# Kernel tuning notes

Hardware: AMD Instinct MI355X
Metric: run time of the kernel (lower is better)

## Reference

```python
import jax, jax.numpy as jnp
import numpy as np

PATCH = 768
POS = 64
HID = 512
B, N = 8, 2048


def setup_inputs() -> dict:
    key = jax.random.key(0)
    ks = jax.random.split(key, 8)
    d_in = PATCH + POS
    s = 1.0 / np.sqrt(d_in)
    return {
        "patches": jax.random.normal(ks[0], (B, N, PATCH), jnp.float32),
        "positions": jax.random.normal(ks[1], (B, N, POS), jnp.float32),
        "Wq": jax.random.uniform(ks[2], (d_in, HID), jnp.float32, -s, s),
        "bq": jax.random.uniform(ks[3], (HID,), jnp.float32, -s, s),
        "Wk": jax.random.uniform(ks[4], (d_in, HID), jnp.float32, -s, s),
        "bk": jax.random.uniform(ks[5], (d_in and HID,), jnp.float32, -s, s),
        "Wv": jax.random.uniform(ks[6], (d_in, HID), jnp.float32, -s, s),
        "bv": jax.random.uniform(ks[7], (HID,), jnp.float32, -s, s),
    }


def reference(patches, positions, Wq, bq, Wk, bk, Wv, bv):
    # concat patch features with positional features: [B, N, PATCH+POS]
    x = jnp.concatenate([patches, positions], axis=-1)
    Q = x @ Wq + bq  # [B, N, HID]
    K = x @ Wk + bk
    V = x @ Wv + bv
    scale = jnp.sqrt(jnp.asarray(HID, x.dtype))
    scores = jnp.einsum("bnd,bmd->bnm", Q, K) / scale  # [B, N, N]
    weights = jax.nn.softmax(scores, axis=-1)
    return jnp.einsum("bnm,bmd->bnd", weights, V)  # [B, N, HID]
```

## Files before the change

kernel.cpp:

```cpp
#include <hip/hip_runtime.h>
#include <hip/hip_bf16.h>
#include <math.h>

typedef __hip_bfloat16 bf16;
typedef __attribute__((ext_vector_type(4))) float f32x4;
typedef __attribute__((ext_vector_type(8))) short s16x8;

typedef const __attribute__((address_space(1))) void gvoid_t;
typedef __attribute__((address_space(3))) void lvoid_t;

__device__ __forceinline__ void gload16(const void* g, void* l) {
  __builtin_amdgcn_global_load_lds((gvoid_t*)g, (lvoid_t*)l, 16, 0, 0);
}
__device__ __forceinline__ unsigned short f2b(float f) {
  bf16 h = __float2bfloat16(f);
  return *(unsigned short*)&h;
}

__global__ __launch_bounds__(256) void prep_x(const float* __restrict__ patches,
                                              const float* __restrict__ positions,
                                              bf16* __restrict__ xb) {
  const long long row = blockIdx.x;
  const int c = threadIdx.x;
  const bool lo = (c < 192);
  const bool hi = (c >= 192) && (c < 208);
  const float* src = lo ? (patches + row * 768 + c * 4)
                        : (positions + row * 64 + (c - 192) * 4);
  if (lo || hi) {
    float4 v = *(const float4*)src;
    const int dst = lo ? (c * 4) : (768 + (c - 192) * 4);
    uint2 w;
    w.x = (unsigned int)f2b(v.x) | ((unsigned int)f2b(v.y) << 16);
    w.y = (unsigned int)f2b(v.z) | ((unsigned int)f2b(v.w) << 16);
    *(uint2*)(xb + row * 832 + dst) = w;
  }
}

__global__ __launch_bounds__(256) void prep_w(const float* __restrict__ Wq,
                                              const float* __restrict__ Wk,
                                              const float* __restrict__ Wv,
                                              bf16* __restrict__ Wt) {
  __shared__ float tile[32][33];
  const int z = blockIdx.z;
  const float* W = (z == 0) ? Wq : (z == 1) ? Wk : Wv;
  bf16* T = Wt + (long long)z * 512 * 832;
  const int n0 = blockIdx.x * 32;
  const int k0 = blockIdx.y * 32;
  const int tx = threadIdx.x, ty = threadIdx.y;
  #pragma unroll
  for (int i = 0; i < 32; i += 8)
    tile[ty + i][tx] = W[(long long)(k0 + ty + i) * 512 + n0 + tx];
  __syncthreads();
  #pragma unroll
  for (int i = 0; i < 32; i += 8)
    T[(long long)(n0 + ty + i) * 832 + k0 + tx] = __float2bfloat16(tile[tx][ty + i]);
}

#define VMW8  asm volatile("s_waitcnt vmcnt(8)" ::: "memory")
#define VMW10 asm volatile("s_waitcnt vmcnt(10)" ::: "memory")
#define PBAR do { __builtin_amdgcn_s_barrier(); __builtin_amdgcn_sched_barrier(0); } while (0)

__device__ __forceinline__ void stage_half(const bf16* src, char* lds, int stride) {
  gload16(src, lds);
  gload16(src + 64 * stride, lds + 8192);
}
__device__ __forceinline__ void lda4(const bf16* base, int rowbase, int llo,
                                     int xk0, int xk1, s16x8 af[4][2]) {
  #pragma unroll
  for (int mf = 0; mf < 4; mf++) {
    const bf16* p = base + (rowbase + mf * 16 + llo) * 64;
    af[mf][0] = *(const s16x8*)(p + xk0);
    af[mf][1] = *(const s16x8*)(p + xk1);
  }
}
__device__ __forceinline__ void ldb2(const bf16* base, int rowbase, int llo,
                                     int xk0, int xk1, s16x8 bfr[2][2]) {
  #pragma unroll
  for (int nf = 0; nf < 2; nf++) {
    const bf16* p = base + (rowbase + nf * 16 + llo) * 64;
    bfr[nf][0] = *(const s16x8*)(p + xk0);
    bfr[nf][1] = *(const s16x8*)(p + xk1);
  }
}
__device__ __forceinline__ void mma16(f32x4 acc[4][2], s16x8 af[4][2],
                                      s16x8 bfr[2][2]) {
  __builtin_amdgcn_s_setprio(1);
  #pragma unroll
  for (int mf = 0; mf < 4; mf++)
    #pragma unroll
    for (int nf = 0; nf < 2; nf++) {
      acc[mf][nf] = __builtin_amdgcn_mfma_f32_16x16x32_bf16(
          af[mf][0], bfr[nf][0], acc[mf][nf], 0, 0, 0);
      acc[mf][nf] = __builtin_amdgcn_mfma_f32_16x16x32_bf16(
          af[mf][1], bfr[nf][1], acc[mf][nf], 0, 0, 0);
    }
  __builtin_amdgcn_s_setprio(0);
}

__global__ __launch_bounds__(512, 2) void gemm_qkv(
    const bf16* __restrict__ xb, const bf16* __restrict__ Wt,
    const float* __restrict__ bq, const float* __restrict__ bk,
    const float* __restrict__ bv,
    bf16* __restrict__ qk, bf16* __restrict__ vt) {
  __shared__ bf16 As[2][256 * 64];
  __shared__ bf16 Bs[2][256 * 64];
  const int tid = threadIdx.x;
  const int wave = tid >> 6, lane = tid & 63;
  const int llo = lane & 15, lhi = lane >> 4;
  const int wm = wave >> 2, wn = wave & 3;

  const unsigned int lin = blockIdx.x;
  const unsigned int xcd = lin & 7u, idx = lin >> 3;
  const unsigned int g = xcd * 48u + idx;
  const unsigned int bm_t = g / 6u;
  const unsigned int bn_t = g - bm_t * 6u;
  const int row0 = (int)bm_t * 256;
  const int col0 = (int)bn_t * 256;
  const int z = col0 >> 9;

  const int sr = tid >> 3;
  const int kkofs = ((tid & 7) ^ (sr & 7)) << 3;
  const bf16* sA = xb + (long long)(row0 + sr) * 832 + kkofs;
  const bf16* sB = Wt + (long long)(col0 + sr) * 832 + kkofs;
  const int wofs = wave * 1024;

  const int xk0 = ((lhi ^ (llo & 7)) << 3);
  const int xk1 = (((4 + lhi) ^ (llo & 7)) << 3);

  f32x4 acc[2][2][4][2] = {};
  s16x8 af[4][2], bf0[2][2], bf1[2][2];

  stage_half(sA, (char*)As[0] + wofs, 832);
  stage_half(sB, (char*)Bs[0] + wofs, 832);
  stage_half(sB + 128 * 832, (char*)Bs[0] + 16384 + wofs, 832);
  stage_half(sA + 128 * 832, (char*)As[0] + 16384 + wofs, 832);
  stage_half(sA + 64, (char*)As[1] + wofs, 832);
  stage_half(sB + 64, (char*)Bs[1] + wofs, 832);
  VMW8; PBAR;

  for (int i = 0; i < 6; ++i) {
    const int kt1 = (2 * i + 1) * 64;
    const int kt2 = (2 * i + 2 <= 12) ? (2 * i + 2) * 64 : 768;
    const int kt3 = (2 * i + 3 <= 12) ? (2 * i + 3) * 64 : 768;
    lda4(As[0], wm * 64, llo, xk0, xk1, af);
    ldb2(Bs[0], wn * 32, llo, xk0, xk1, bf0);
    stage_half(sB + 128 * 832 + kt1, (char*)Bs[1] + 16384 + wofs, 832);
    VMW8; PBAR;
    mma16(acc[0][0], af, bf0);
    ldb2(Bs[0], 128 + wn * 32, llo, xk0, xk1, bf1);
    stage_half(sA + 128 * 832 + kt1, (char*)As[1] + 16384 + wofs, 832);
    VMW8; PBAR;
    mma16(acc[0][1], af, bf1);
    lda4(As[0], 128 + wm * 64, llo, xk0, xk1, af);
    stage_half(sA + kt2, (char*)As[0] + wofs, 832);
    PBAR;
    mma16(acc[1][0], af, bf0);
    stage_half(sB + kt2, (char*)Bs[0] + wofs, 832);
    VMW8; PBAR;
    mma16(acc[1][1], af, bf1);
    lda4(As[1], wm * 64, llo, xk0, xk1, af);
    ldb2(Bs[1], wn * 32, llo, xk0, xk1, bf0);
    stage_half(sB + 128 * 832 + kt2, (char*)Bs[0] + 16384 + wofs, 832);
    VMW8; PBAR;
    mma16(acc[0][0], af, bf0);
    ldb2(Bs[1], 128 + wn * 32, llo, xk0, xk1, bf1);
    stage_half(sA + 128 * 832 + kt2, (char*)As[0] + 16384 + wofs, 832);
    VMW8; PBAR;
    mma16(acc[0][1], af, bf1);
    lda4(As[1], 128 + wm * 64, llo, xk0, xk1, af);
    stage_half(sA + kt3, (char*)As[1] + wofs, 832);
    PBAR;
    mma16(acc[1][0], af, bf0);
    stage_half(sB + kt3, (char*)Bs[1] + wofs, 832);
    VMW8; PBAR;
    mma16(acc[1][1], af, bf1);
  }

  asm volatile("s_waitcnt vmcnt(4)" ::: "memory");
  PBAR;
  lda4(As[0], wm * 64, llo, xk0, xk1, af);
  ldb2(Bs[0], wn * 32, llo, xk0, xk1, bf0);
  ldb2(Bs[0], 128 + wn * 32, llo, xk0, xk1, bf1);
  mma16(acc[0][0], af, bf0);
  mma16(acc[0][1], af, bf1);
  lda4(As[0], 128 + wm * 64, llo, xk0, xk1, af);
  mma16(acc[1][0], af, bf0);
  mma16(acc[1][1], af, bf1);
  asm volatile("s_waitcnt vmcnt(0)" ::: "memory");

  if (z < 2) {
    const float* bias = z ? bk : bq;
    bf16* outp = qk + (long long)z * 16384 * 512;
    #pragma unroll
    for (int qr = 0; qr < 2; qr++)
      #pragma unroll
      for (int qc = 0; qc < 2; qc++)
        #pragma unroll
        for (int mf = 0; mf < 4; mf++)
          #pragma unroll
          for (int nf = 0; nf < 2; nf++) {
            const int c = (col0 & 511) + qc * 128 + wn * 32 + nf * 16 + llo;
            const int grow0 = row0 + qr * 128 + wm * 64 + mf * 16 + lhi * 4;
            const float bb = bias[c];
            #pragma unroll
            for (int r = 0; r < 4; r++)
              outp[(long long)(grow0 + r) * 512 + c] =
                  __float2bfloat16(acc[qr][qc][mf][nf][r] + bb);
          }
  } else {
    #pragma unroll
    for (int qr = 0; qr < 2; qr++)
      #pragma unroll
      for (int qc = 0; qc < 2; qc++)
        #pragma unroll
        for (int mf = 0; mf < 4; mf++)
          #pragma unroll
          for (int nf = 0; nf < 2; nf++) {
            const int c = (col0 & 511) + qc * 128 + wn * 32 + nf * 16 + llo;
            const int grow0 = row0 + qr * 128 + wm * 64 + mf * 16 + lhi * 4;
            const int b = grow0 >> 11, j = grow0 & 2047;
            const float bb = bv[c];
            uint2 w;
            w.x = (unsigned int)f2b(acc[qr][qc][mf][nf][0] + bb) |
                  ((unsigned int)f2b(acc[qr][qc][mf][nf][1] + bb) << 16);
            w.y = (unsigned int)f2b(acc[qr][qc][mf][nf][2] + bb) |
                  ((unsigned int)f2b(acc[qr][qc][mf][nf][3] + bb) << 16);
            *(uint2*)(vt + (long long)b * 512 * 2048 + (long long)c * 2048 + j) = w;
          }
  }
}

__global__ __launch_bounds__(512, 2) void gemm_scores(const bf16* __restrict__ qk,
                                                      bf16* __restrict__ S,
                                                      float* __restrict__ rowsumP) {
  __shared__ bf16 As[2][256 * 64];
  __shared__ bf16 Bs[2][256 * 64];
  const int tid = threadIdx.x;
  const int wave = tid >> 6, lane = tid & 63;
  const int llo = lane & 15, lhi = lane >> 4;
  const int wm = wave >> 2, wn = wave & 3;

  const unsigned int lin = blockIdx.x;
  const int b = (int)(lin & 7u);
  const unsigned int idx = lin >> 3;
  const int row0 = (int)(idx >> 3) * 256;
  const int coltile = (int)(idx & 7u);
  const int col0 = coltile * 256;

  const bf16* Ab = qk + (long long)b * 2048 * 512;
  const bf16* Bb = qk + (long long)16384 * 512 + (long long)b * 2048 * 512;

  const int sr = tid >> 3;
  const int kkofs = ((tid & 7) ^ (sr & 7)) << 3;
  const bf16* sA = Ab + (long long)(row0 + sr) * 512 + kkofs;
  const bf16* sB = Bb + (long long)(col0 + sr) * 512 + kkofs;
  const int wofs = wave * 1024;

  const int xk0 = ((lhi ^ (llo & 7)) << 3);
  const int xk1 = (((4 + lhi) ^ (llo & 7)) << 3);

  f32x4 acc[2][2][4][2] = {};
  s16x8 af[4][2], bf0[2][2], bf1[2][2];

  stage_half(sA, (char*)As[0] + wofs, 512);
  stage_half(sB, (char*)Bs[0] + wofs, 512);
  stage_half(sB + 128 * 512, (char*)Bs[0] + 16384 + wofs, 512);
  stage_half(sA + 128 * 512, (char*)As[0] + 16384 + wofs, 512);
  stage_half(sA + 64, (char*)As[1] + wofs, 512);
  stage_half(sB + 64, (char*)Bs[1] + wofs, 512);
  VMW8; PBAR;

  for (int i = 0; i < 4; ++i) {
    const int kt1 = (2 * i + 1) * 64;
    const int kt2 = (2 * i + 2 < 8) ? (2 * i + 2) * 64 : 448;
    const int kt3 = (2 * i + 3 < 8) ? (2 * i + 3) * 64 : 448;
    lda4(As[0], wm * 64, llo, xk0, xk1, af);
    ldb2(Bs[0], wn * 32, llo, xk0, xk1, bf0);
    stage_half(sB + 128 * 512 + kt1, (char*)Bs[1] + 16384 + wofs, 512);
    VMW8; PBAR;
    mma16(acc[0][0], af, bf0);
    ldb2(Bs[0], 128 + wn * 32, llo, xk0, xk1, bf1);
    stage_half(sA + 128 * 512 + kt1, (char*)As[1] + 16384 + wofs, 512);
    VMW8; PBAR;
    mma16(acc[0][1], af, bf1);
    lda4(As[0], 128 + wm * 64, llo, xk0, xk1, af);
    stage_half(sA + kt2, (char*)As[0] + wofs, 512);
    PBAR;
    mma16(acc[1][0], af, bf0);
    stage_half(sB + kt2, (char*)Bs[0] + wofs, 512);
    VMW8; PBAR;
    mma16(acc[1][1], af, bf1);
    lda4(As[1], wm * 64, llo, xk0, xk1, af);
    ldb2(Bs[1], wn * 32, llo, xk0, xk1, bf0);
    stage_half(sB + 128 * 512 + kt2, (char*)Bs[0] + 16384 + wofs, 512);
    VMW8; PBAR;
    mma16(acc[0][0], af, bf0);
    ldb2(Bs[1], 128 + wn * 32, llo, xk0, xk1, bf1);
    stage_half(sA + 128 * 512 + kt2, (char*)As[0] + 16384 + wofs, 512);
    VMW8; PBAR;
    mma16(acc[0][1], af, bf1);
    lda4(As[1], 128 + wm * 64, llo, xk0, xk1, af);
    stage_half(sA + kt3, (char*)As[1] + wofs, 512);
    PBAR;
    mma16(acc[1][0], af, bf0);
    stage_half(sB + kt3, (char*)Bs[1] + wofs, 512);
    VMW8; PBAR;
    mma16(acc[1][1], af, bf1);
  }

  __syncthreads();

  const float alpha = 0.044194173824159216f;
  bf16* Sb = S + (long long)b * 2048 * 2048;
  #pragma unroll
  for (int qr = 0; qr < 2; qr++)
    #pragma unroll
    for (int qc = 0; qc < 2; qc++)
      #pragma unroll
      for (int mf = 0; mf < 4; mf++)
        #pragma unroll
        for (int nf = 0; nf < 2; nf++) {
          #pragma unroll
          for (int r = 0; r < 4; r++)
            acc[qr][qc][mf][nf][r] = __expf(acc[qr][qc][mf][nf][r] * alpha);
          const int gcol = col0 + qc * 128 + wn * 32 + nf * 16 + llo;
          const int grow0 = row0 + qr * 128 + wm * 64 + mf * 16 + lhi * 4;
          #pragma unroll
          for (int r = 0; r < 4; r++)
            Sb[(long long)(grow0 + r) * 2048 + gcol] =
                __float2bfloat16(acc[qr][qc][mf][nf][r]);
        }

  float* psum = (float*)As;
  #pragma unroll
  for (int qr = 0; qr < 2; qr++)
    #pragma unroll
    for (int mf = 0; mf < 4; mf++)
      #pragma unroll
      for (int r = 0; r < 4; r++) {
        float p = acc[qr][0][mf][0][r] + acc[qr][0][mf][1][r] +
                  acc[qr][1][mf][0][r] + acc[qr][1][mf][1][r];
        p += __shfl_xor(p, 1, 64);
        p += __shfl_xor(p, 2, 64);
        p += __shfl_xor(p, 4, 64);
        p += __shfl_xor(p, 8, 64);
        if (llo == 0)
          psum[wn * 256 + qr * 128 + wm * 64 + mf * 16 + lhi * 4 + r] = p;
      }
  __syncthreads();
  if (tid < 256) {
    const float v = psum[tid] + psum[256 + tid] + psum[512 + tid] + psum[768 + tid];
    rowsumP[(long long)(b * 8 + coltile) * 2048 + row0 + tid] = v;
  }
}

__global__ __launch_bounds__(256) void reduce_rowsum(
    const float* __restrict__ rowsumP, float* __restrict__ rinv) {
  const int i = blockIdx.x * 256 + threadIdx.x;
  const int b = i >> 11, row = i & 2047;
  const float* p = rowsumP + ((long long)b * 8) * 2048 + row;
  float s = 0.f;
  #pragma unroll
  for (int t = 0; t < 8; t++) s += p[t * 2048];
  rinv[i] = 1.0f / s;
}

#define PV_TILE(c, cs, kstage)                                              \
  do {                                                                      \
                                                              \
    lda4(As3[c], wm * 64, llo, xk0, xk1, af);                               \
    ldb2(Bs3[c], wn * 32, llo, xk0, xk1, bfr);                              \
    stage_half(sA + (kstage), (char*)As3[cs] + wofs, 2048);                 \
    stage_half(sB + (kstage), (char*)Bs3[cs] + wofs, 2048);                 \
    VMW10; PBAR;                                                            \
    mma16(acc[0], af, bfr);                                                 \
                              \
    lda4(As3[c], 128 + wm * 64, llo, xk0, xk1, af);                         \
    stage_half(sA + 128 * 2048 + (kstage), (char*)As3[cs] + 16384 + wofs,   \
               2048);                                                       \
    VMW8; PBAR;                                                             \
    mma16(acc[1], af, bfr);                                                 \
  } while (0)

__global__ __launch_bounds__(512, 2) void gemm_pv(const bf16* __restrict__ S,
                                                  const bf16* __restrict__ vt,
                                                  const float* __restrict__ rinv,
                                                  float* __restrict__ out) {
  __shared__ bf16 As3[3][256 * 64];
  __shared__ bf16 Bs3[3][128 * 64];
  const int tid = threadIdx.x;
  const int wave = tid >> 6, lane = tid & 63;
  const int llo = lane & 15, lhi = lane >> 4;
  const int wm = wave >> 2, wn = wave & 3;

  const unsigned int lin = blockIdx.x;
  const int b = (int)(lin & 7u);
  const unsigned int idx = lin >> 3;
  const int row0 = (int)(idx >> 2) * 256;
  const int col0 = (int)(idx & 3u) * 128;

  const bf16* Ab = S + (long long)b * 2048 * 2048;
  const bf16* Bb = vt + (long long)b * 512 * 2048;

  const int sr = tid >> 3;
  const int kkofs = ((tid & 7) ^ (sr & 7)) << 3;
  const bf16* sA = Ab + (long long)(row0 + sr) * 2048 + kkofs;
  const bf16* sB = Bb + (long long)(col0 + sr) * 2048 + kkofs;
  const int wofs = wave * 1024;

  const int xk0 = ((lhi ^ (llo & 7)) << 3);
  const int xk1 = (((4 + lhi) ^ (llo & 7)) << 3);

  f32x4 acc[2][4][2] = {};
  s16x8 af[4][2], bfr[2][2];

  stage_half(sA, (char*)As3[0] + wofs, 2048);
  stage_half(sB, (char*)Bs3[0] + wofs, 2048);
  stage_half(sA + 128 * 2048, (char*)As3[0] + 16384 + wofs, 2048);
  stage_half(sA + 64, (char*)As3[1] + wofs, 2048);
  stage_half(sB + 64, (char*)Bs3[1] + wofs, 2048);
  stage_half(sA + 128 * 2048 + 64, (char*)As3[1] + 16384 + wofs, 2048);
  VMW8; PBAR;

  for (int j = 0; j < 10; ++j) {
    const int kb = j * 192;
    PV_TILE(0, 2, kb + 128);
    PV_TILE(1, 0, kb + 192);
    PV_TILE(2, 1, kb + 256);
  }
  PV_TILE(0, 2, 1984);
  PV_TILE(1, 0, 1984);

  asm volatile("s_waitcnt vmcnt(0)" ::: "memory");

  const float* rs = rinv + (long long)b * 2048;
  float* Ob = out + (long long)b * 2048 * 512;
  #pragma unroll
  for (int qr = 0; qr < 2; qr++)
    #pragma unroll
    for (int mf = 0; mf < 4; mf++) {
      const int grow0 = row0 + qr * 128 + wm * 64 + mf * 16 + lhi * 4;
      float iv[4];
      #pragma unroll
      for (int r = 0; r < 4; r++) iv[r] = rs[grow0 + r];
      #pragma unroll
      for (int nf = 0; nf < 2; nf++) {
        const int gcol = col0 + wn * 32 + nf * 16 + llo;
        #pragma unroll
        for (int r = 0; r < 4; r++)
          Ob[(long long)(grow0 + r) * 512 + gcol] = acc[qr][mf][nf][r] * iv[r];
      }
    }
}
#undef PV_TILE

extern "C" void kernel_launch(void* const* d_in, const int* in_sizes, int n_in,
                              void* d_out, int out_size, void* d_ws, size_t ws_size,
                              hipStream_t stream) {
  const float* patches = (const float*)d_in[0];
  const float* positions = (const float*)d_in[1];
  const float* Wq = (const float*)d_in[2];
  const float* bq = (const float*)d_in[3];
  const float* Wk = (const float*)d_in[4];
  const float* bk = (const float*)d_in[5];
  const float* Wv = (const float*)d_in[6];
  const float* bv = (const float*)d_in[7];
  float* out = (float*)d_out;

  if (ws_size < 149422080u) return;

  char* ws = (char*)d_ws;
  bf16* Wt = (bf16*)(ws);
  bf16* xb = (bf16*)(ws + 2555904);
  bf16* qk = (bf16*)(ws + 29818880);
  bf16* vt = (bf16*)(ws + 63373312);
  bf16* S  = (bf16*)(ws + 80150528);
  float* rinv    = (float*)(ws + 147259392);
  float* rowsumP = (float*)(ws + 147324928);

  prep_x<<<16384, 256, 0, stream>>>(patches, positions, xb);
  prep_w<<<dim3(16, 26, 3), dim3(32, 8), 0, stream>>>(Wq, Wk, Wv, Wt);
  gemm_qkv<<<384, 512, 0, stream>>>(xb, Wt, bq, bk, bv, qk, vt);
  gemm_scores<<<512, 512, 0, stream>>>(qk, S, rowsumP);
  reduce_rowsum<<<64, 256, 0, stream>>>(rowsumP, rinv);
  gemm_pv<<<256, 512, 0, stream>>>(S, vt, rinv, out);
}
```

Measured before the change: 264.0 us.

## Retile QKV GEMM to 256x192 tiles with triple-buffered B

The QKV projection GEMM goes from 256x256 output tiles (384 blocks) to 256x192 tiles (512 blocks). This fills all CUs evenly, two blocks per CU. B tiles now use a 3-stage LDS ring and A stays double-buffered, with a new macro-driven pipeline and waitcnt depth. A tile can now span the Q/K/V boundary, so the epilogue picks the output and bias per column. Separately, prep_x converts 8 rows per block instead of one, which cuts the launch to 2048 blocks.

```diff
diff --git a/kernel.cpp b/kernel.cpp
--- a/kernel.cpp
+++ b/kernel.cpp
@@ -20,15 +20,17 @@
 __global__ __launch_bounds__(256) void prep_x(const float* __restrict__ patches,
                                               const float* __restrict__ positions,
                                               bf16* __restrict__ xb) {
-  const long long row = blockIdx.x;
   const int c = threadIdx.x;
   const bool lo = (c < 192);
   const bool hi = (c >= 192) && (c < 208);
-  const float* src = lo ? (patches + row * 768 + c * 4)
-                        : (positions + row * 64 + (c - 192) * 4);
-  if (lo || hi) {
+  if (!(lo || hi)) return;
+  const int dst = lo ? (c * 4) : (768 + (c - 192) * 4);
+  #pragma unroll
+  for (int rr = 0; rr < 8; ++rr) {
+    const long long row = (long long)blockIdx.x * 8 + rr;
+    const float* src = lo ? (patches + row * 768 + c * 4)
+                          : (positions + row * 64 + (c - 192) * 4);
     float4 v = *(const float4*)src;
-    const int dst = lo ? (c * 4) : (768 + (c - 192) * 4);
     uint2 w;
     w.x = (unsigned int)f2b(v.x) | ((unsigned int)f2b(v.y) << 16);
     w.y = (unsigned int)f2b(v.z) | ((unsigned int)f2b(v.w) << 16);
@@ -56,6 +58,7 @@
     T[(long long)(n0 + ty + i) * 832 + k0 + tx] = __float2bfloat16(tile[tx][ty + i]);
 }
 
+#define VMW5  asm volatile("s_waitcnt vmcnt(5)" ::: "memory")
 #define VMW8  asm volatile("s_waitcnt vmcnt(8)" ::: "memory")
 #define VMW10 asm volatile("s_waitcnt vmcnt(10)" ::: "memory")
 #define PBAR do { __builtin_amdgcn_s_barrier(); __builtin_amdgcn_sched_barrier(0); } while (0)
@@ -63,6 +66,11 @@
 __device__ __forceinline__ void stage_half(const bf16* src, char* lds, int stride) {
   gload16(src, lds);
   gload16(src + 64 * stride, lds + 8192);
+}
+__device__ __forceinline__ void stage_b192(const bf16* src, char* lds) {
+  gload16(src, lds);
+  gload16(src + 64 * 832, lds + 8192);
+  gload16(src + 128 * 832, lds + 16384);
 }
 __device__ __forceinline__ void lda4(const bf16* base, int rowbase, int llo,
                                      int xk0, int xk1, s16x8 af[4][2]) {
@@ -77,6 +85,15 @@
                                      int xk0, int xk1, s16x8 bfr[2][2]) {
   #pragma unroll
   for (int nf = 0; nf < 2; nf++) {
+    const bf16* p = base + (rowbase + nf * 16 + llo) * 64;
+    bfr[nf][0] = *(const s16x8*)(p + xk0);
+    bfr[nf][1] = *(const s16x8*)(p + xk1);
+  }
+}
+__device__ __forceinline__ void ldb3(const bf16* base, int rowbase, int llo,
+                                     int xk0, int xk1, s16x8 bfr[3][2]) {
+  #pragma unroll
+  for (int nf = 0; nf < 3; nf++) {
     const bf16* p = base + (rowbase + nf * 16 + llo) * 64;
     bfr[nf][0] = *(const s16x8*)(p + xk0);
     bfr[nf][1] = *(const s16x8*)(p + xk1);
@@ -96,14 +113,45 @@
     }
   __builtin_amdgcn_s_setprio(0);
 }
+__device__ __forceinline__ void mma24(f32x4 acc[4][3], s16x8 af[4][2],
+                                      s16x8 bfr[3][2]) {
+  __builtin_amdgcn_s_setprio(1);
+  #pragma unroll
+  for (int mf = 0; mf < 4; mf++)
+    #pragma unroll
+    for (int nf = 0; nf < 3; nf++) {
+      acc[mf][nf] = __builtin_amdgcn_mfma_f32_16x16x32_bf16(
+          af[mf][0], bfr[nf][0], acc[mf][nf], 0, 0, 0);
+      acc[mf][nf] = __builtin_amdgcn_mfma_f32_16x16x32_bf16(
+          af[mf][1], bfr[nf][1], acc[mf][nf], 0, 0, 0);
+    }
+  __builtin_amdgcn_s_setprio(0);
+}
+
+#define QKV_TILE(abuf, bbuf, bstage, ka1, kb2)                               \
+  do {                                                                       \
+                                                               \
+    lda4(As2[abuf], wm * 64, llo, xk0, xk1, af);                             \
+    ldb3(Bs3[bbuf], wn * 48, llo, xk0, xk1, bfr);                            \
+    stage_half(sA + (ka1), (char*)As2[(abuf) ^ 1] + wofs, 832);              \
+    stage_b192(sB + (kb2), (char*)Bs3[bstage] + wofs);                       \
+    VMW5; PBAR;                                                              \
+    mma24(acc[0], af, bfr);                                                  \
+                               \
+    lda4(As2[abuf], 128 + wm * 64, llo, xk0, xk1, af);                       \
+    stage_half(sA + 128 * 832 + (ka1), (char*)As2[(abuf) ^ 1] + 16384 + wofs,\
+               832);                                                         \
+    VMW5; PBAR;                                                              \
+    mma24(acc[1], af, bfr);                                                  \
+  } while (0)
 
 __global__ __launch_bounds__(512, 2) void gemm_qkv(
     const bf16* __restrict__ xb, const bf16* __restrict__ Wt,
     const float* __restrict__ bq, const float* __restrict__ bk,
     const float* __restrict__ bv,
     bf16* __restrict__ qk, bf16* __restrict__ vt) {
-  __shared__ bf16 As[2][256 * 64];
-  __shared__ bf16 Bs[2][256 * 64];
+  __shared__ bf16 As2[2][256 * 64];
+  __shared__ bf16 Bs3[3][192 * 64];
   const int tid = threadIdx.x;
   const int wave = tid >> 6, lane = tid & 63;
   const int llo = lane & 15, lhi = lane >> 4;
@@ -111,12 +159,11 @@
 
   const unsigned int lin = blockIdx.x;
   const unsigned int xcd = lin & 7u, idx = lin >> 3;
-  const unsigned int g = xcd * 48u + idx;
-  const unsigned int bm_t = g / 6u;
-  const unsigned int bn_t = g - bm_t * 6u;
-  const int row0 = (int)bm_t * 256;
-  const int col0 = (int)bn_t * 256;
-  const int z = col0 >> 9;
+  const unsigned int g = xcd * 64u + idx;
+  const int bm_t = (int)(g >> 3);
+  const int bn_t = (int)(g & 7u);
+  const int row0 = bm_t * 256;
+  const int col0 = bn_t * 192;
 
   const int sr = tid >> 3;
   const int kkofs = ((tid & 7) ^ (sr & 7)) << 3;
@@ -127,108 +174,57 @@
   const int xk0 = ((lhi ^ (llo & 7)) << 3);
   const int xk1 = (((4 + lhi) ^ (llo & 7)) << 3);
 
-  f32x4 acc[2][2][4][2] = {};
-  s16x8 af[4][2], bf0[2][2], bf1[2][2];
-
-  stage_half(sA, (char*)As[0] + wofs, 832);
-  stage_half(sB, (char*)Bs[0] + wofs, 832);
-  stage_half(sB + 128 * 832, (char*)Bs[0] + 16384 + wofs, 832);
-  stage_half(sA + 128 * 832, (char*)As[0] + 16384 + wofs, 832);
-  stage_half(sA + 64, (char*)As[1] + wofs, 832);
-  stage_half(sB + 64, (char*)Bs[1] + wofs, 832);
-  VMW8; PBAR;
-
-  for (int i = 0; i < 6; ++i) {
-    const int kt1 = (2 * i + 1) * 64;
-    const int kt2 = (2 * i + 2 <= 12) ? (2 * i + 2) * 64 : 768;
-    const int kt3 = (2 * i + 3 <= 12) ? (2 * i + 3) * 64 : 768;
-    lda4(As[0], wm * 64, llo, xk0, xk1, af);
-    ldb2(Bs[0], wn * 32, llo, xk0, xk1, bf0);
-    stage_half(sB + 128 * 832 + kt1, (char*)Bs[1] + 16384 + wofs, 832);
-    VMW8; PBAR;
-    mma16(acc[0][0], af, bf0);
-    ldb2(Bs[0], 128 + wn * 32, llo, xk0, xk1, bf1);
-    stage_half(sA + 128 * 832 + kt1, (char*)As[1] + 16384 + wofs, 832);
-    VMW8; PBAR;
-    mma16(acc[0][1], af, bf1);
-    lda4(As[0], 128 + wm * 64, llo, xk0, xk1, af);
-    stage_half(sA + kt2, (char*)As[0] + wofs, 832);
-    PBAR;
-    mma16(acc[1][0], af, bf0);
-    stage_half(sB + kt2, (char*)Bs[0] + wofs, 832);
-    VMW8; PBAR;
-    mma16(acc[1][1], af, bf1);
-    lda4(As[1], wm * 64, llo, xk0, xk1, af);
-    ldb2(Bs[1], wn * 32, llo, xk0, xk1, bf0);
-    stage_half(sB + 128 * 832 + kt2, (char*)Bs[0] + 16384 + wofs, 832);
-    VMW8; PBAR;
-    mma16(acc[0][0], af, bf0);
-    ldb2(Bs[1], 128 + wn * 32, llo, xk0, xk1, bf1);
-    stage_half(sA + 128 * 832 + kt2, (char*)As[0] + 16384 + wofs, 832);
-    VMW8; PBAR;
-    mma16(acc[0][1], af, bf1);
-    lda4(As[1], 128 + wm * 64, llo, xk0, xk1, af);
-    stage_half(sA + kt3, (char*)As[1] + wofs, 832);
-    PBAR;
-    mma16(acc[1][0], af, bf0);
-    stage_half(sB + kt3, (char*)Bs[1] + wofs, 832);
-    VMW8; PBAR;
-    mma16(acc[1][1], af, bf1);
-  }
-
-  asm volatile("s_waitcnt vmcnt(4)" ::: "memory");
-  PBAR;
-  lda4(As[0], wm * 64, llo, xk0, xk1, af);
-  ldb2(Bs[0], wn * 32, llo, xk0, xk1, bf0);
-  ldb2(Bs[0], 128 + wn * 32, llo, xk0, xk1, bf1);
-  mma16(acc[0][0], af, bf0);
-  mma16(acc[0][1], af, bf1);
-  lda4(As[0], 128 + wm * 64, llo, xk0, xk1, af);
-  mma16(acc[1][0], af, bf0);
-  mma16(acc[1][1], af, bf1);
+  f32x4 acc[2][4][3] = {};
+  s16x8 af[4][2], bfr[3][2];
+
+  stage_half(sA, (char*)As2[0] + wofs, 832);
+  stage_b192(sB, (char*)Bs3[0] + wofs);
+  stage_half(sA + 128 * 832, (char*)As2[0] + 16384 + wofs, 832);
+  stage_b192(sB + 64, (char*)Bs3[1] + wofs);
+  VMW5; PBAR;
+
+  for (int jj = 0; jj < 2; ++jj) {
+    const int u0 = jj * 6;
+    QKV_TILE(0, 0, 2, (u0 + 1) * 64, (u0 + 2) * 64);
+    QKV_TILE(1, 1, 0, (u0 + 2) * 64, (u0 + 3) * 64);
+    QKV_TILE(0, 2, 1, (u0 + 3) * 64, (u0 + 4) * 64);
+    QKV_TILE(1, 0, 2, (u0 + 4) * 64, (u0 + 5) * 64);
+    QKV_TILE(0, 1, 0, (u0 + 5) * 64, (u0 + 6) * 64);
+    QKV_TILE(1, 2, 1, (u0 + 6) * 64, ((u0 + 7) <= 12 ? (u0 + 7) * 64 : 768));
+  }
+  QKV_TILE(0, 0, 2, 768, 768);
+
   asm volatile("s_waitcnt vmcnt(0)" ::: "memory");
 
-  if (z < 2) {
-    const float* bias = z ? bk : bq;
-    bf16* outp = qk + (long long)z * 16384 * 512;
-    #pragma unroll
-    for (int qr = 0; qr < 2; qr++)
+  #pragma unroll
+  for (int qr = 0; qr < 2; qr++)
+    #pragma unroll
+    for (int mf = 0; mf < 4; mf++)
       #pragma unroll
-      for (int qc = 0; qc < 2; qc++)
-        #pragma unroll
-        for (int mf = 0; mf < 4; mf++)
+      for (int nf = 0; nf < 3; nf++) {
+        const int c = col0 + wn * 48 + nf * 16 + llo;
+        const int z = c >> 9, cc = c & 511;
+        const int grow0 = row0 + qr * 128 + wm * 64 + mf * 16 + lhi * 4;
+        if (z < 2) {
+          const float bb = (z ? bk : bq)[cc];
+          bf16* outp = qk + (long long)z * 16384 * 512;
           #pragma unroll
-          for (int nf = 0; nf < 2; nf++) {
-            const int c = (col0 & 511) + qc * 128 + wn * 32 + nf * 16 + llo;
-            const int grow0 = row0 + qr * 128 + wm * 64 + mf * 16 + lhi * 4;
-            const float bb = bias[c];
-            #pragma unroll
-            for (int r = 0; r < 4; r++)
-              outp[(long long)(grow0 + r) * 512 + c] =
-                  __float2bfloat16(acc[qr][qc][mf][nf][r] + bb);
-          }
-  } else {
-    #pragma unroll
-    for (int qr = 0; qr < 2; qr++)
-      #pragma unroll
-      for (int qc = 0; qc < 2; qc++)
-        #pragma unroll
-        for (int mf = 0; mf < 4; mf++)
-          #pragma unroll
-          for (int nf = 0; nf < 2; nf++) {
-            const int c = (col0 & 511) + qc * 128 + wn * 32 + nf * 16 + llo;
-            const int grow0 = row0 + qr * 128 + wm * 64 + mf * 16 + lhi * 4;
-            const int b = grow0 >> 11, j = grow0 & 2047;
-            const float bb = bv[c];
-            uint2 w;
-            w.x = (unsigned int)f2b(acc[qr][qc][mf][nf][0] + bb) |
-                  ((unsigned int)f2b(acc[qr][qc][mf][nf][1] + bb) << 16);
-            w.y = (unsigned int)f2b(acc[qr][qc][mf][nf][2] + bb) |
-                  ((unsigned int)f2b(acc[qr][qc][mf][nf][3] + bb) << 16);
-            *(uint2*)(vt + (long long)b * 512 * 2048 + (long long)c * 2048 + j) = w;
-          }
-  }
-}
+          for (int r = 0; r < 4; r++)
+            outp[(long long)(grow0 + r) * 512 + cc] =
+                __float2bfloat16(acc[qr][mf][nf][r] + bb);
+        } else {
+          const int b = grow0 >> 11, j = grow0 & 2047;
+          const float bb = bv[cc];
+          uint2 w;
+          w.x = (unsigned int)f2b(acc[qr][mf][nf][0] + bb) |
+                ((unsigned int)f2b(acc[qr][mf][nf][1] + bb) << 16);
+          w.y = (unsigned int)f2b(acc[qr][mf][nf][2] + bb) |
+                ((unsigned int)f2b(acc[qr][mf][nf][3] + bb) << 16);
+          *(uint2*)(vt + (long long)b * 512 * 2048 + (long long)cc * 2048 + j) = w;
+        }
+      }
+}
+#undef QKV_TILE
 
 __global__ __launch_bounds__(512, 2) void gemm_scores(const bf16* __restrict__ qk,
                                                       bf16* __restrict__ S,
@@ -478,9 +474,9 @@
   float* rinv    = (float*)(ws + 147259392);
   float* rowsumP = (float*)(ws + 147324928);
 
-  prep_x<<<16384, 256, 0, stream>>>(patches, positions, xb);
+  prep_x<<<2048, 256, 0, stream>>>(patches, positions, xb);
   prep_w<<<dim3(16, 26, 3), dim3(32, 8), 0, stream>>>(Wq, Wk, Wv, Wt);
-  gemm_qkv<<<384, 512, 0, stream>>>(xb, Wt, bq, bk, bv, qk, vt);
+  gemm_qkv<<<512, 512, 0, stream>>>(xb, Wt, bq, bk, bv, qk, vt);
   gemm_scores<<<512, 512, 0, stream>>>(qk, S, rowsumP);
   reduce_rowsum<<<64, 256, 0, stream>>>(rowsumP, rinv);
   gemm_pv<<<256, 512, 0, stream>>>(S, vt, rinv, out);
```

Result: no change. 262.1 us (-0.7%).
